# Kernel tuning notes

Measured on AMD Instinct MI355X. Metric: run time of the kernel, lower is better.

Reference implementation:

```python
import jax, jax.numpy as jnp
import numpy as np

EPS = 1e-08

def setup_inputs() -> dict:
    key = jax.random.key(0)
    x = jax.random.normal(key, (16, 2048), dtype=jnp.float32)  # [B, L]
    return {"x": x}

def reference(x) -> jnp.ndarray:
    # min-max normalize per series to [-1, 1]
    min_x = jnp.min(x, axis=1, keepdims=True)
    max_x = jnp.max(x, axis=1, keepdims=True)
    scaled = 2.0 * ((x - min_x) / (max_x - min_x + EPS)) - 1.0
    scaled = jnp.clip(scaled, -1.0 + EPS, 1.0 - EPS)
    phi = jnp.arccos(scaled)                      # [B, L]
    gaf = jnp.cos(phi[:, :, None] + phi[:, None, :])  # [B, L, L]
    return gaf
```

## Files before the change

### kernel.cpp

```cpp
#include <hip/hip_runtime.h>
#include <math.h>

#define L 2048
#define NB 16
#define ROWS_PER_BLOCK 16
#define THREADS 256
#define GAF_EPS 1e-8f

typedef float f32x4 __attribute__((ext_vector_type(4)));

__global__ __launch_bounds__(THREADS) void gaf_kernel(const float* __restrict__ x,
                                                      float* __restrict__ out) {
    __shared__ float sc[L];
    __shared__ float ss[L];
    __shared__ float red[8];

    const int chunks_per_batch = L / ROWS_PER_BLOCK;
    const int b = blockIdx.x / chunks_per_batch;
    const int i0 = (blockIdx.x % chunks_per_batch) * ROWS_PER_BLOCK;
    const int t = threadIdx.x;
    const float* __restrict__ xrow = x + (size_t)b * L;

    float v[8];
    float mn = INFINITY, mx = -INFINITY;
#pragma unroll
    for (int k = 0; k < 8; ++k) {
        v[k] = xrow[t + k * THREADS];
        mn = fminf(mn, v[k]);
        mx = fmaxf(mx, v[k]);
    }
#pragma unroll
    for (int off = 32; off > 0; off >>= 1) {
        mn = fminf(mn, __shfl_xor(mn, off));
        mx = fmaxf(mx, __shfl_xor(mx, off));
    }
    const int wave = t >> 6;
    if ((t & 63) == 0) { red[wave] = mn; red[4 + wave] = mx; }
    __syncthreads();
    mn = fminf(fminf(red[0], red[1]), fminf(red[2], red[3]));
    mx = fmaxf(fmaxf(red[4], red[5]), fmaxf(red[6], red[7]));
    const float inv = 1.0f / (mx - mn + GAF_EPS);

#pragma unroll
    for (int k = 0; k < 8; ++k) {
        float c = 2.0f * ((v[k] - mn) * inv) - 1.0f;
        c = fminf(fmaxf(c, -1.0f + GAF_EPS), 1.0f - GAF_EPS);
        const int idx = t + k * THREADS;
        sc[idx] = c;
        ss[idx] = sqrtf(fmaxf(1.0f - c * c, 0.0f));
    }
    __syncthreads();

    float ci[ROWS_PER_BLOCK], si[ROWS_PER_BLOCK];
#pragma unroll
    for (int i = 0; i < ROWS_PER_BLOCK; ++i) {
        ci[i] = sc[i0 + i];
        si[i] = ss[i0 + i];
    }

    float* __restrict__ obase = out + ((size_t)b * L + (size_t)i0) * L;
#pragma unroll
    for (int it = 0; it < L / (4 * THREADS); ++it) {
        const int j4 = t + it * THREADS;
        const f32x4 cj = ((const f32x4*)sc)[j4];
        const f32x4 sj = ((const f32x4*)ss)[j4];
#pragma unroll
        for (int i = 0; i < ROWS_PER_BLOCK; ++i) {
            f32x4 o;
            o.x = ci[i] * cj.x - si[i] * sj.x;
            o.y = ci[i] * cj.y - si[i] * sj.y;
            o.z = ci[i] * cj.z - si[i] * sj.z;
            o.w = ci[i] * cj.w - si[i] * sj.w;
            __builtin_nontemporal_store(o, (f32x4*)(obase + (size_t)i * L) + j4);
        }
    }
}

extern "C" void kernel_launch(void* const* d_in, const int* in_sizes, int n_in,
                              void* d_out, int out_size, void* d_ws, size_t ws_size,
                              hipStream_t stream) {
    const float* x = (const float*)d_in[0];
    float* out = (float*)d_out;
    const dim3 grid(NB * (L / ROWS_PER_BLOCK));
    gaf_kernel<<<grid, THREADS, 0, stream>>>(x, out);
}
```

Measured before the change: 262.3 us.

## Use fewer larger blocks with per-thread column registers and broadcast row loads

Reorganizes the grid so each 512-thread block covers 128 rows of a batch instead of 16. Each thread keeps its four columns' cos/sin values in registers and reads the row values from shared memory as broadcasts. This amortizes the per-block min/max reduction and normalization prologue over more output. The trade-off is far fewer blocks (one per CU), which may reduce memory-level parallelism for the store-bound output.

```diff
diff --git a/kernel.cpp b/kernel.cpp
--- a/kernel.cpp
+++ b/kernel.cpp
@@ -3,8 +3,9 @@
 
 #define L 2048
 #define NB 16
-#define ROWS_PER_BLOCK 16
-#define THREADS 256
+#define THREADS 512
+#define BLOCKS_PER_BATCH 16
+#define ROWS_PER_BLOCK (L / BLOCKS_PER_BATCH)
 #define GAF_EPS 1e-8f
 
 typedef float f32x4 __attribute__((ext_vector_type(4)));
@@ -13,66 +14,65 @@
                                                       float* __restrict__ out) {
     __shared__ float sc[L];
     __shared__ float ss[L];
-    __shared__ float red[8];
+    __shared__ float red[16];
 
-    const int chunks_per_batch = L / ROWS_PER_BLOCK;
-    const int b = blockIdx.x / chunks_per_batch;
-    const int i0 = (blockIdx.x % chunks_per_batch) * ROWS_PER_BLOCK;
+    const int b = blockIdx.x / BLOCKS_PER_BATCH;
+    const int q = blockIdx.x % BLOCKS_PER_BATCH;
     const int t = threadIdx.x;
-    const float* __restrict__ xrow = x + (size_t)b * L;
 
-    float v[8];
-    float mn = INFINITY, mx = -INFINITY;
-#pragma unroll
-    for (int k = 0; k < 8; ++k) {
-        v[k] = xrow[t + k * THREADS];
-        mn = fminf(mn, v[k]);
-        mx = fmaxf(mx, v[k]);
-    }
+    const f32x4 v = ((const f32x4*)(x + (size_t)b * L))[t];
+    float mn = fminf(fminf(v.x, v.y), fminf(v.z, v.w));
+    float mx = fmaxf(fmaxf(v.x, v.y), fmaxf(v.z, v.w));
+
 #pragma unroll
     for (int off = 32; off > 0; off >>= 1) {
         mn = fminf(mn, __shfl_xor(mn, off));
         mx = fmaxf(mx, __shfl_xor(mx, off));
     }
     const int wave = t >> 6;
-    if ((t & 63) == 0) { red[wave] = mn; red[4 + wave] = mx; }
+    if ((t & 63) == 0) { red[wave] = mn; red[8 + wave] = mx; }
     __syncthreads();
-    mn = fminf(fminf(red[0], red[1]), fminf(red[2], red[3]));
-    mx = fmaxf(fmaxf(red[4], red[5]), fmaxf(red[6], red[7]));
+    mn = red[0];
+    mx = red[8];
+#pragma unroll
+    for (int w = 1; w < 8; ++w) {
+        mn = fminf(mn, red[w]);
+        mx = fmaxf(mx, red[8 + w]);
+    }
     const float inv = 1.0f / (mx - mn + GAF_EPS);
 
+    f32x4 c4, s4;
+    {
+        float cv[4] = {v.x, v.y, v.z, v.w};
 #pragma unroll
-    for (int k = 0; k < 8; ++k) {
-        float c = 2.0f * ((v[k] - mn) * inv) - 1.0f;
-        c = fminf(fmaxf(c, -1.0f + GAF_EPS), 1.0f - GAF_EPS);
-        const int idx = t + k * THREADS;
-        sc[idx] = c;
-        ss[idx] = sqrtf(fmaxf(1.0f - c * c, 0.0f));
+        for (int k = 0; k < 4; ++k) {
+            float c = 2.0f * ((cv[k] - mn) * inv) - 1.0f;
+            c = fminf(fmaxf(c, -1.0f + GAF_EPS), 1.0f - GAF_EPS);
+            cv[k] = c;
+        }
+        c4.x = cv[0]; c4.y = cv[1]; c4.z = cv[2]; c4.w = cv[3];
+        s4.x = sqrtf(fmaxf(1.0f - c4.x * c4.x, 0.0f));
+        s4.y = sqrtf(fmaxf(1.0f - c4.y * c4.y, 0.0f));
+        s4.z = sqrtf(fmaxf(1.0f - c4.z * c4.z, 0.0f));
+        s4.w = sqrtf(fmaxf(1.0f - c4.w * c4.w, 0.0f));
     }
+    ((f32x4*)sc)[t] = c4;
+    ((f32x4*)ss)[t] = s4;
     __syncthreads();
 
-    float ci[ROWS_PER_BLOCK], si[ROWS_PER_BLOCK];
-#pragma unroll
-    for (int i = 0; i < ROWS_PER_BLOCK; ++i) {
-        ci[i] = sc[i0 + i];
-        si[i] = ss[i0 + i];
-    }
-
-    float* __restrict__ obase = out + ((size_t)b * L + (size_t)i0) * L;
-#pragma unroll
-    for (int it = 0; it < L / (4 * THREADS); ++it) {
-        const int j4 = t + it * THREADS;
-        const f32x4 cj = ((const f32x4*)sc)[j4];
-        const f32x4 sj = ((const f32x4*)ss)[j4];
-#pragma unroll
-        for (int i = 0; i < ROWS_PER_BLOCK; ++i) {
-            f32x4 o;
-            o.x = ci[i] * cj.x - si[i] * sj.x;
-            o.y = ci[i] * cj.y - si[i] * sj.y;
-            o.z = ci[i] * cj.z - si[i] * sj.z;
-            o.w = ci[i] * cj.w - si[i] * sj.w;
-            __builtin_nontemporal_store(o, (f32x4*)(obase + (size_t)i * L) + j4);
-        }
+    float* __restrict__ obase =
+        out + ((size_t)b * L + (size_t)q * ROWS_PER_BLOCK) * L;
+#pragma unroll 8
+    for (int m = 0; m < ROWS_PER_BLOCK; ++m) {
+        const int r = q * ROWS_PER_BLOCK + m;
+        const float ci = sc[r];
+        const float si = ss[r];
+        f32x4 o;
+        o.x = ci * c4.x - si * s4.x;
+        o.y = ci * c4.y - si * s4.y;
+        o.z = ci * c4.z - si * s4.z;
+        o.w = ci * c4.w - si * s4.w;
+        __builtin_nontemporal_store(o, (f32x4*)(obase + (size_t)m * L) + t);
     }
 }
 
@@ -81,6 +81,6 @@
                               hipStream_t stream) {
     const float* x = (const float*)d_in[0];
     float* out = (float*)d_out;
-    const dim3 grid(NB * (L / ROWS_PER_BLOCK));
+    const dim3 grid(NB * BLOCKS_PER_BATCH);
     gaf_kernel<<<grid, THREADS, 0, stream>>>(x, out);
 }
```

Result: no change. 260.6 us (median of 2 runs) (-0.7%).
